# Kernel tuning notes

Hardware: AMD Instinct MI355X
Metric: run time of the kernel (lower is better)

## Reference

```python
import jax, jax.numpy as jnp
import numpy as np

B = 65536        # batch_size
F = 128          # feature_dim (shared-layer output)
H = 256          # hidden dim of each domain tower
D = 8            # num_domains
OUT = 1          # per-domain tower output dim


def setup_inputs() -> dict:
    key = jax.random.key(0)
    k_x, k_w1, k_b1, k_w2, k_b2, k_id = jax.random.split(key, 6)
    x = jax.random.normal(k_x, (B, F), dtype=jnp.float32)
    select_domain_ids = jax.random.randint(k_id, (B,), 0, D)
    # stacked per-domain MLP params (one tower per domain)
    s1 = 1.0 / np.sqrt(F)
    s2 = 1.0 / np.sqrt(H)
    W1 = jax.random.uniform(k_w1, (D, F, H), minval=-s1, maxval=s1, dtype=jnp.float32)
    b1 = jax.random.uniform(k_b1, (D, H), minval=-s1, maxval=s1, dtype=jnp.float32)
    W2 = jax.random.uniform(k_w2, (D, H, OUT), minval=-s2, maxval=s2, dtype=jnp.float32)
    b2 = jax.random.uniform(k_b2, (D, OUT), minval=-s2, maxval=s2, dtype=jnp.float32)
    return {"x": x, "select_domain_ids": select_domain_ids,
            "W1": W1, "b1": b1, "W2": W2, "b2": b2}


def reference(x, select_domain_ids, W1, b1, W2, b2):
    # Run EVERY domain tower on the full batch (dense compute), as the
    # original module does, then gather the selected domain per sample.
    h = jax.nn.relu(jnp.einsum('bf,dfh->bdh', x, W1) + b1)      # [B, D, H]
    logits = jnp.einsum('bdh,dho->bdo', h, W2) + b2             # [B, D, OUT]
    # domain_select: logits[arange(B), domain_ids] -> [B, OUT]
    out = jnp.take_along_axis(logits, select_domain_ids[:, None, None], axis=1)[:, 0]
    return out
```

## Files before the change

### kernel.cpp

```cpp
#include <hip/hip_runtime.h>
#include <hip/hip_bf16.h>

#define BN 65536
#define FD 128
#define HD 256
#define DN 8
#define NB 256
#define TM 128
#define MAXT (BN / TM + DN)

typedef float f32x4 __attribute__((ext_vector_type(4)));
using bf16x8 = __attribute__((ext_vector_type(8))) __bf16;

union BF8 { bf16x8 v; unsigned short u[8]; };

__device__ __forceinline__ unsigned short f2bf(float f) {
  unsigned int x = __float_as_uint(f);
  x += 0x7fffu + ((x >> 16) & 1u);
  return (unsigned short)(x >> 16);
}

__global__ void kw(const float* __restrict__ W1, unsigned short* __restrict__ W1T) {
  int o = blockIdx.x * 256 + threadIdx.x;
  int d = o >> 15;
  int rem = o & 32767;
  int h = rem >> 7;
  int f = rem & 127;
  W1T[o] = f2bf(W1[(d * FD + f) * HD + h]);
}

__global__ void k1(const int* __restrict__ ids, int* __restrict__ local_pos,
                   int* __restrict__ cnt_blk) {
  __shared__ int hist[DN];
  int t = threadIdx.x;
  if (t < DN) hist[t] = 0;
  __syncthreads();
  int i = blockIdx.x * 256 + t;
  int id = ids[i];
  local_pos[i] = atomicAdd(&hist[id], 1);
  __syncthreads();
  if (t < DN) cnt_blk[blockIdx.x * DN + t] = hist[t];
}

__global__ void k2(const int* __restrict__ cnt_blk, int* __restrict__ blk_base,
                   int* __restrict__ dom_off, int* __restrict__ tile_d,
                   int* __restrict__ tile_start, int* __restrict__ tile_rows,
                   int* __restrict__ n_tiles) {
  __shared__ int s_cnt[DN], s_off[DN], s_T[DN + 1];
  int t = threadIdx.x;
  int d = t >> 6;
  int l = t & 63;
  int c[4];
  int sum = 0;
#pragma unroll
  for (int j = 0; j < 4; j++) { c[j] = cnt_blk[(l * 4 + j) * DN + d]; sum += c[j]; }
  int run = sum;
  for (int off = 1; off < 64; off <<= 1) {
    int v = __shfl_up(run, off);
    if (l >= off) run += v;
  }
  int excl = run - sum;
#pragma unroll
  for (int j = 0; j < 4; j++) { blk_base[(l * 4 + j) * DN + d] = excl; excl += c[j]; }
  if (l == 63) s_cnt[d] = run;
  __syncthreads();
  if (t == 0) {
    int off = 0, T = 0;
    for (int dd = 0; dd < DN; dd++) {
      s_off[dd] = off; dom_off[dd] = off; off += s_cnt[dd];
      s_T[dd] = T; T += (s_cnt[dd] + TM - 1) / TM;
    }
    s_T[DN] = T;
    *n_tiles = T;
  }
  __syncthreads();
  int T = s_T[DN];
  for (int tt = t; tt < T; tt += 512) {
    int dd = 0;
    while (s_T[dd + 1] <= tt) dd++;
    int k = tt - s_T[dd];
    tile_d[tt] = dd;
    tile_start[tt] = s_off[dd] + k * TM;
    tile_rows[tt] = min(TM, s_cnt[dd] - k * TM);
  }
}

__global__ void k3(const int* __restrict__ ids, const int* __restrict__ local_pos,
                   const int* __restrict__ blk_base, const int* __restrict__ dom_off,
                   int* __restrict__ perm) {
  __shared__ int base[DN];
  int t = threadIdx.x;
  if (t < DN) base[t] = dom_off[t] + blk_base[blockIdx.x * DN + t];
  __syncthreads();
  int i = blockIdx.x * 256 + t;
  perm[base[ids[i]] + local_pos[i]] = i;
}

__global__ __launch_bounds__(512) void kmain(
    const float* __restrict__ x, const float* __restrict__ b1,
    const float* __restrict__ W2, const float* __restrict__ b2,
    const unsigned short* __restrict__ W1T, const int* __restrict__ perm,
    const int* __restrict__ tile_d, const int* __restrict__ tile_start,
    const int* __restrict__ tile_rows, const int* __restrict__ n_tiles,
    float* __restrict__ out) {
  int bid = blockIdx.x;
  if (bid >= *n_tiles) return;
  int d = tile_d[bid];
  int start = tile_start[bid];
  int rows = tile_rows[bid];

  __shared__ int s_perm[TM];
  __shared__ float s_red[TM][2];

  int t = threadIdx.x;
  if (t < TM) s_perm[t] = perm[start + min(t, rows - 1)];
  __syncthreads();

  int lane = t & 63;
  int wave = t >> 6;
  int nhalf = wave >> 2;
  int mbase = (wave & 3) * 32;
  int lg = lane >> 4;
  int lr = lane & 15;

  const unsigned short* Wd = W1T + (size_t)d * HD * FD;
  const float* xr0 = x + (size_t)s_perm[mbase + lr] * FD;
  const float* xr1 = x + (size_t)s_perm[mbase + 16 + lr] * FD;

  f32x4 acc[2][8];
#pragma unroll
  for (int mt = 0; mt < 2; mt++)
#pragma unroll
    for (int nt = 0; nt < 8; nt++) acc[mt][nt] = (f32x4){0.f, 0.f, 0.f, 0.f};

#pragma unroll
  for (int ks = 0; ks < 4; ks++) {
    int k0 = ks * 32 + lg * 8;
    BF8 a0, a1;
    f32x4 u0 = *(const f32x4*)(xr0 + k0);
    f32x4 u1 = *(const f32x4*)(xr0 + k0 + 4);
    f32x4 v0 = *(const f32x4*)(xr1 + k0);
    f32x4 v1 = *(const f32x4*)(xr1 + k0 + 4);
#pragma unroll
    for (int j = 0; j < 4; j++) {
      a0.u[j] = f2bf(u0[j]); a0.u[4 + j] = f2bf(u1[j]);
      a1.u[j] = f2bf(v0[j]); a1.u[4 + j] = f2bf(v1[j]);
    }
#pragma unroll
    for (int nt = 0; nt < 8; nt++) {
      int n = nhalf * 128 + nt * 16 + lr;
      bf16x8 bf = *(const bf16x8*)(Wd + (size_t)n * FD + k0);
      acc[0][nt] = __builtin_amdgcn_mfma_f32_16x16x32_bf16(a0.v, bf, acc[0][nt], 0, 0, 0);
      acc[1][nt] = __builtin_amdgcn_mfma_f32_16x16x32_bf16(a1.v, bf, acc[1][nt], 0, 0, 0);
    }
  }

  float part[2][4] = {{0.f, 0.f, 0.f, 0.f}, {0.f, 0.f, 0.f, 0.f}};
#pragma unroll
  for (int nt = 0; nt < 8; nt++) {
    int c = nhalf * 128 + nt * 16 + lr;
    float b1v = b1[d * HD + c];
    float w2v = W2[d * HD + c];
#pragma unroll
    for (int mt = 0; mt < 2; mt++)
#pragma unroll
      for (int q = 0; q < 4; q++) {
        float h = acc[mt][nt][q] + b1v;
        h = h > 0.f ? h : 0.f;
        part[mt][q] = fmaf(h, w2v, part[mt][q]);
      }
  }
#pragma unroll
  for (int off = 1; off < 16; off <<= 1)
#pragma unroll
    for (int mt = 0; mt < 2; mt++)
#pragma unroll
      for (int q = 0; q < 4; q++)
        part[mt][q] += __shfl_xor(part[mt][q], off);

  if (lr == 0) {
#pragma unroll
    for (int mt = 0; mt < 2; mt++)
#pragma unroll
      for (int q = 0; q < 4; q++) {
        int r = mbase + mt * 16 + lg * 4 + q;
        s_red[r][nhalf] = part[mt][q];
      }
  }
  __syncthreads();
  if (t < rows) out[s_perm[t]] = s_red[t][0] + s_red[t][1] + b2[d];
}

extern "C" void kernel_launch(void* const* d_in, const int* in_sizes, int n_in,
                              void* d_out, int out_size, void* d_ws, size_t ws_size,
                              hipStream_t stream) {
  const float* x   = (const float*)d_in[0];
  const int*   ids = (const int*)d_in[1];
  const float* W1  = (const float*)d_in[2];
  const float* b1  = (const float*)d_in[3];
  const float* W2  = (const float*)d_in[4];
  const float* b2  = (const float*)d_in[5];
  float* out = (float*)d_out;

  int* ws = (int*)d_ws;
  int* perm       = ws;
  int* local_pos  = ws + 65536;
  int* cnt_blk    = ws + 131072;
  int* blk_base   = ws + 133120;
  int* dom_off    = ws + 135168;
  int* tile_d     = ws + 135200;
  int* tile_start = ws + 135760;
  int* tile_rows  = ws + 136320;
  int* n_tiles    = ws + 136880;
  unsigned short* W1T = (unsigned short*)((char*)d_ws + 640u * 1024u);

  hipLaunchKernelGGL(kw, dim3(DN * FD * HD / 256), dim3(256), 0, stream, W1, W1T);
  hipLaunchKernelGGL(k1, dim3(NB), dim3(256), 0, stream, ids, local_pos, cnt_blk);
  hipLaunchKernelGGL(k2, dim3(1), dim3(512), 0, stream, cnt_blk, blk_base, dom_off,
                     tile_d, tile_start, tile_rows, n_tiles);
  hipLaunchKernelGGL(k3, dim3(NB), dim3(256), 0, stream, ids, local_pos, blk_base,
                     dom_off, perm);
  hipLaunchKernelGGL(kmain, dim3(MAXT), dim3(512), 0, stream, x, b1, W2, b2, W1T,
                     perm, tile_d, tile_start, tile_rows, n_tiles, out);
}
```

Measured before the change: 124.6 us.

## Fuse preprocessing into one kernel and use persistent slot-based grouped GEMM

Collapses the W1 transpose, histogram, scan and scatter kernels into a single pre-kernel. It uses global atomics to build per-domain buckets of fixed capacity, and the W1 transpose now goes through LDS so reads and writes are coalesced. The main kernel becomes a grid-strided loop over domain/tile slots with 64-row tiles, and the x tile is staged in swizzled LDS as bf16. Each wave handles a 32-column slice, with an 8-way reduction at the end. This removes several launches and the serial scan, at the cost of nondeterministic row ordering within each domain and a larger perm buffer.

```diff
diff --git a/kernel.cpp b/kernel.cpp
--- a/kernel.cpp
+++ b/kernel.cpp
@@ -5,14 +5,13 @@
 #define FD 128
 #define HD 256
 #define DN 8
-#define NB 256
-#define TM 128
-#define MAXT (BN / TM + DN)
+#define TM 64
+#define SLOTS 8192
+#define GRID_MAIN 2048
 
 typedef float f32x4 __attribute__((ext_vector_type(4)));
 using bf16x8 = __attribute__((ext_vector_type(8))) __bf16;
-
-union BF8 { bf16x8 v; unsigned short u[8]; };
+typedef unsigned short us4 __attribute__((ext_vector_type(4)));
 
 __device__ __forceinline__ unsigned short f2bf(float f) {
   unsigned int x = __float_as_uint(f);
@@ -20,175 +19,152 @@
   return (unsigned short)(x >> 16);
 }
 
-__global__ void kw(const float* __restrict__ W1, unsigned short* __restrict__ W1T) {
-  int o = blockIdx.x * 256 + threadIdx.x;
-  int d = o >> 15;
-  int rem = o & 32767;
-  int h = rem >> 7;
-  int f = rem & 127;
-  W1T[o] = f2bf(W1[(d * FD + f) * HD + h]);
-}
+__global__ __launch_bounds__(256) void k_pre(
+    const float* __restrict__ W1, const int* __restrict__ ids,
+    unsigned short* __restrict__ W1T, int* __restrict__ g_cnt,
+    int* __restrict__ perm) {
+  __shared__ int hist[DN], base[DN];
+  __shared__ unsigned short tile[64][136];
+  int t = threadIdx.x, bid = blockIdx.x;
 
-__global__ void k1(const int* __restrict__ ids, int* __restrict__ local_pos,
-                   int* __restrict__ cnt_blk) {
-  __shared__ int hist[DN];
-  int t = threadIdx.x;
   if (t < DN) hist[t] = 0;
   __syncthreads();
-  int i = blockIdx.x * 256 + t;
+  int i = bid * 256 + t;
   int id = ids[i];
-  local_pos[i] = atomicAdd(&hist[id], 1);
+  int lp = atomicAdd(&hist[id], 1);
   __syncthreads();
-  if (t < DN) cnt_blk[blockIdx.x * DN + t] = hist[t];
-}
+  if (t < DN) base[t] = atomicAdd(&g_cnt[t], hist[t]);
+  __syncthreads();
+  perm[(id << 16) + base[id] + lp] = i;
 
-__global__ void k2(const int* __restrict__ cnt_blk, int* __restrict__ blk_base,
-                   int* __restrict__ dom_off, int* __restrict__ tile_d,
-                   int* __restrict__ tile_start, int* __restrict__ tile_rows,
-                   int* __restrict__ n_tiles) {
-  __shared__ int s_cnt[DN], s_off[DN], s_T[DN + 1];
-  int t = threadIdx.x;
-  int d = t >> 6;
-  int l = t & 63;
-  int c[4];
-  int sum = 0;
+  if (bid < 32) {
+    int db = bid >> 2, hb = bid & 3;
+    int fr = t >> 4, hq = t & 15;
+    const float* src = W1 + (size_t)db * FD * HD + hb * 64 + hq * 4;
 #pragma unroll
-  for (int j = 0; j < 4; j++) { c[j] = cnt_blk[(l * 4 + j) * DN + d]; sum += c[j]; }
-  int run = sum;
-  for (int off = 1; off < 64; off <<= 1) {
-    int v = __shfl_up(run, off);
-    if (l >= off) run += v;
-  }
-  int excl = run - sum;
+    for (int jj = 0; jj < 8; jj++) {
+      int f = fr + 16 * jj;
+      f32x4 v = *(const f32x4*)(src + (size_t)f * HD);
 #pragma unroll
-  for (int j = 0; j < 4; j++) { blk_base[(l * 4 + j) * DN + d] = excl; excl += c[j]; }
-  if (l == 63) s_cnt[d] = run;
-  __syncthreads();
-  if (t == 0) {
-    int off = 0, T = 0;
-    for (int dd = 0; dd < DN; dd++) {
-      s_off[dd] = off; dom_off[dd] = off; off += s_cnt[dd];
-      s_T[dd] = T; T += (s_cnt[dd] + TM - 1) / TM;
+      for (int e = 0; e < 4; e++) tile[hq * 4 + e][f] = f2bf(v[e]);
     }
-    s_T[DN] = T;
-    *n_tiles = T;
-  }
-  __syncthreads();
-  int T = s_T[DN];
-  for (int tt = t; tt < T; tt += 512) {
-    int dd = 0;
-    while (s_T[dd + 1] <= tt) dd++;
-    int k = tt - s_T[dd];
-    tile_d[tt] = dd;
-    tile_start[tt] = s_off[dd] + k * TM;
-    tile_rows[tt] = min(TM, s_cnt[dd] - k * TM);
+    __syncthreads();
+    unsigned short* dst = W1T + (size_t)db * HD * FD + (size_t)hb * 64 * FD;
+    int h = t >> 2, c = t & 3;
+#pragma unroll
+    for (int j = 0; j < 4; j++) {
+      int f = c * 32 + j * 8;
+      *(us4*)(dst + h * FD + f)     = *(const us4*)&tile[h][f];
+      *(us4*)(dst + h * FD + f + 4) = *(const us4*)&tile[h][f + 4];
+    }
   }
 }
 
-__global__ void k3(const int* __restrict__ ids, const int* __restrict__ local_pos,
-                   const int* __restrict__ blk_base, const int* __restrict__ dom_off,
-                   int* __restrict__ perm) {
-  __shared__ int base[DN];
-  int t = threadIdx.x;
-  if (t < DN) base[t] = dom_off[t] + blk_base[blockIdx.x * DN + t];
-  __syncthreads();
-  int i = blockIdx.x * 256 + t;
-  perm[base[ids[i]] + local_pos[i]] = i;
-}
-
-__global__ __launch_bounds__(512) void kmain(
+__global__ __launch_bounds__(512, 4) void kmain(
     const float* __restrict__ x, const float* __restrict__ b1,
     const float* __restrict__ W2, const float* __restrict__ b2,
     const unsigned short* __restrict__ W1T, const int* __restrict__ perm,
-    const int* __restrict__ tile_d, const int* __restrict__ tile_start,
-    const int* __restrict__ tile_rows, const int* __restrict__ n_tiles,
-    float* __restrict__ out) {
-  int bid = blockIdx.x;
-  if (bid >= *n_tiles) return;
-  int d = tile_d[bid];
-  int start = tile_start[bid];
-  int rows = tile_rows[bid];
+    const int* __restrict__ g_cnt, float* __restrict__ out) {
+  __shared__ unsigned short xs[TM * FD];
+  __shared__ float s_red[TM][8];
+  int t = threadIdx.x;
 
-  __shared__ int s_perm[TM];
-  __shared__ float s_red[TM][2];
+  for (int s = blockIdx.x; s < SLOTS; s += GRID_MAIN) {
+    int d = s & 7, k = s >> 3;
+    int rows = g_cnt[d] - k * TM;
+    if (rows <= 0) continue;
+    rows = min(rows, TM);
+    const int* pr = perm + (d << 16) + k * TM;
+    const unsigned short* Wd = W1T + (size_t)d * HD * FD;
 
-  int t = threadIdx.x;
-  if (t < TM) s_perm[t] = perm[start + min(t, rows - 1)];
-  __syncthreads();
+    {
+      int r = t >> 3, c8 = t & 7;
+      int gi = pr[min(r, rows - 1)];
+      const float* xr = x + (size_t)gi * FD;
+      f32x4 v[4];
+#pragma unroll
+      for (int j = 0; j < 4; j++) v[j] = *(const f32x4*)(xr + (c8 + 8 * j) * 4);
+#pragma unroll
+      for (int j = 0; j < 4; j++) {
+        int fc = c8 + 8 * j;
+        int us = (r * FD + fc * 4) ^ ((r & 7) << 3);
+        us4 wv;
+        wv[0] = f2bf(v[j][0]); wv[1] = f2bf(v[j][1]);
+        wv[2] = f2bf(v[j][2]); wv[3] = f2bf(v[j][3]);
+        *(us4*)&xs[us] = wv;
+      }
+    }
+    __syncthreads();
 
-  int lane = t & 63;
-  int wave = t >> 6;
-  int nhalf = wave >> 2;
-  int mbase = (wave & 3) * 32;
-  int lg = lane >> 4;
-  int lr = lane & 15;
-
-  const unsigned short* Wd = W1T + (size_t)d * HD * FD;
-  const float* xr0 = x + (size_t)s_perm[mbase + lr] * FD;
-  const float* xr1 = x + (size_t)s_perm[mbase + 16 + lr] * FD;
-
-  f32x4 acc[2][8];
+    int lane = t & 63, w = t >> 6;
+    int lg = lane >> 4, lr = lane & 15;
+    int colbase = w * 32;
+    f32x4 acc[4][2];
 #pragma unroll
-  for (int mt = 0; mt < 2; mt++)
+    for (int mf = 0; mf < 4; mf++)
 #pragma unroll
-    for (int nt = 0; nt < 8; nt++) acc[mt][nt] = (f32x4){0.f, 0.f, 0.f, 0.f};
+      for (int nt = 0; nt < 2; nt++) acc[mf][nt] = (f32x4){0.f, 0.f, 0.f, 0.f};
 
 #pragma unroll
-  for (int ks = 0; ks < 4; ks++) {
-    int k0 = ks * 32 + lg * 8;
-    BF8 a0, a1;
-    f32x4 u0 = *(const f32x4*)(xr0 + k0);
-    f32x4 u1 = *(const f32x4*)(xr0 + k0 + 4);
-    f32x4 v0 = *(const f32x4*)(xr1 + k0);
-    f32x4 v1 = *(const f32x4*)(xr1 + k0 + 4);
+    for (int ks = 0; ks < 4; ks++) {
+      bf16x8 a[4];
 #pragma unroll
-    for (int j = 0; j < 4; j++) {
-      a0.u[j] = f2bf(u0[j]); a0.u[4 + j] = f2bf(u1[j]);
-      a1.u[j] = f2bf(v0[j]); a1.u[4 + j] = f2bf(v1[j]);
+      for (int mf = 0; mf < 4; mf++) {
+        int row = mf * 16 + lr;
+        int us = (row * FD + ks * 32 + lg * 8) ^ ((row & 7) << 3);
+        a[mf] = *(const bf16x8*)&xs[us];
+      }
+#pragma unroll
+      for (int nt = 0; nt < 2; nt++) {
+        int col = colbase + nt * 16 + lr;
+        bf16x8 bfrag = *(const bf16x8*)(Wd + (size_t)col * FD + ks * 32 + lg * 8);
+#pragma unroll
+        for (int mf = 0; mf < 4; mf++)
+          acc[mf][nt] = __builtin_amdgcn_mfma_f32_16x16x32_bf16(a[mf], bfrag, acc[mf][nt], 0, 0, 0);
+      }
+    }
+
+    float part[4][4];
+#pragma unroll
+    for (int mf = 0; mf < 4; mf++)
+#pragma unroll
+      for (int q = 0; q < 4; q++) part[mf][q] = 0.f;
+#pragma unroll
+    for (int nt = 0; nt < 2; nt++) {
+      int col = colbase + nt * 16 + lr;
+      float b1v = b1[d * HD + col];
+      float w2v = W2[d * HD + col];
+#pragma unroll
+      for (int mf = 0; mf < 4; mf++)
+#pragma unroll
+        for (int q = 0; q < 4; q++) {
+          float h = acc[mf][nt][q] + b1v;
+          h = h > 0.f ? h : 0.f;
+          part[mf][q] = fmaf(h, w2v, part[mf][q]);
+        }
     }
 #pragma unroll
-    for (int nt = 0; nt < 8; nt++) {
-      int n = nhalf * 128 + nt * 16 + lr;
-      bf16x8 bf = *(const bf16x8*)(Wd + (size_t)n * FD + k0);
-      acc[0][nt] = __builtin_amdgcn_mfma_f32_16x16x32_bf16(a0.v, bf, acc[0][nt], 0, 0, 0);
-      acc[1][nt] = __builtin_amdgcn_mfma_f32_16x16x32_bf16(a1.v, bf, acc[1][nt], 0, 0, 0);
+    for (int off = 1; off < 16; off <<= 1)
+#pragma unroll
+      for (int mf = 0; mf < 4; mf++)
+#pragma unroll
+        for (int q = 0; q < 4; q++)
+          part[mf][q] += __shfl_xor(part[mf][q], off);
+    if (lr == 0) {
+#pragma unroll
+      for (int mf = 0; mf < 4; mf++)
+#pragma unroll
+        for (int q = 0; q < 4; q++)
+          s_red[mf * 16 + lg * 4 + q][w] = part[mf][q];
     }
+    __syncthreads();
+    if (t < rows) {
+      const float* sr = s_red[t];
+      out[pr[t]] = sr[0] + sr[1] + sr[2] + sr[3] + sr[4] + sr[5] + sr[6] + sr[7]
+                   + b2[d];
+    }
+    __syncthreads();
   }
-
-  float part[2][4] = {{0.f, 0.f, 0.f, 0.f}, {0.f, 0.f, 0.f, 0.f}};
-#pragma unroll
-  for (int nt = 0; nt < 8; nt++) {
-    int c = nhalf * 128 + nt * 16 + lr;
-    float b1v = b1[d * HD + c];
-    float w2v = W2[d * HD + c];
-#pragma unroll
-    for (int mt = 0; mt < 2; mt++)
-#pragma unroll
-      for (int q = 0; q < 4; q++) {
-        float h = acc[mt][nt][q] + b1v;
-        h = h > 0.f ? h : 0.f;
-        part[mt][q] = fmaf(h, w2v, part[mt][q]);
-      }
-  }
-#pragma unroll
-  for (int off = 1; off < 16; off <<= 1)
-#pragma unroll
-    for (int mt = 0; mt < 2; mt++)
-#pragma unroll
-      for (int q = 0; q < 4; q++)
-        part[mt][q] += __shfl_xor(part[mt][q], off);
-
-  if (lr == 0) {
-#pragma unroll
-    for (int mt = 0; mt < 2; mt++)
-#pragma unroll
-      for (int q = 0; q < 4; q++) {
-        int r = mbase + mt * 16 + lg * 4 + q;
-        s_red[r][nhalf] = part[mt][q];
-      }
-  }
-  __syncthreads();
-  if (t < rows) out[s_perm[t]] = s_red[t][0] + s_red[t][1] + b2[d];
 }
 
 extern "C" void kernel_launch(void* const* d_in, const int* in_sizes, int n_in,
@@ -202,24 +178,14 @@
   const float* b2  = (const float*)d_in[5];
   float* out = (float*)d_out;
 
-  int* ws = (int*)d_ws;
-  int* perm       = ws;
-  int* local_pos  = ws + 65536;
-  int* cnt_blk    = ws + 131072;
-  int* blk_base   = ws + 133120;
-  int* dom_off    = ws + 135168;
-  int* tile_d     = ws + 135200;
-  int* tile_start = ws + 135760;
-  int* tile_rows  = ws + 136320;
-  int* n_tiles    = ws + 136880;
-  unsigned short* W1T = (unsigned short*)((char*)d_ws + 640u * 1024u);
+  char* ws = (char*)d_ws;
+  int* g_cnt = (int*)ws;
+  int* perm  = (int*)(ws + 1024);
+  unsigned short* W1T = (unsigned short*)(ws + 1024 + (size_t)DN * BN * 4);
 
-  hipLaunchKernelGGL(kw, dim3(DN * FD * HD / 256), dim3(256), 0, stream, W1, W1T);
-  hipLaunchKernelGGL(k1, dim3(NB), dim3(256), 0, stream, ids, local_pos, cnt_blk);
-  hipLaunchKernelGGL(k2, dim3(1), dim3(512), 0, stream, cnt_blk, blk_base, dom_off,
-                     tile_d, tile_start, tile_rows, n_tiles);
-  hipLaunchKernelGGL(k3, dim3(NB), dim3(256), 0, stream, ids, local_pos, blk_base,
-                     dom_off, perm);
-  hipLaunchKernelGGL(kmain, dim3(MAXT), dim3(512), 0, stream, x, b1, W2, b2, W1T,
-                     perm, tile_d, tile_start, tile_rows, n_tiles, out);
+  hipMemsetAsync(g_cnt, 0, DN * sizeof(int), stream);
+  hipLaunchKernelGGL(k_pre, dim3(BN / 256), dim3(256), 0, stream,
+                     W1, ids, W1T, g_cnt, perm);
+  hipLaunchKernelGGL(kmain, dim3(GRID_MAIN), dim3(512), 0, stream,
+                     x, b1, W2, b2, W1T, perm, g_cnt, out);
 }
```

New measurement: 105.3 us. 1.18x faster.
